# Optimization experiments

Hardware: AMD Instinct MI355X
Metric: run time of the kernel (lower is better)

The kernel has to match this reference:

```python
import jax, jax.numpy as jnp
import numpy as np
from jax import lax

DN = ('NHWC', 'HWIO', 'NHWC')

def _conv(x, k, b, stride=1):
    return lax.conv_general_dilated(x, k, (stride, stride), 'SAME', dimension_numbers=DN) + b

def _tconv(x, k, b):
    return lax.conv_transpose(x, k, (2, 2), 'SAME', dimension_numbers=DN) + b


def setup_inputs() -> dict:
    key = jax.random.key(0)
    ks = jax.random.split(key, 32)
    ki = iter(ks)
    def w(shape, scale=0.05):
        return (jax.random.normal(next(ki), shape, dtype=jnp.float32) * scale)
    inp = {}
    inp['x'] = jax.random.uniform(next(ki), (8, 128, 128, 3), dtype=jnp.float32)
    # encoder
    inp['k1'],  inp['b1']  = w((11, 11, 3, 32)),   jnp.zeros((32,), jnp.float32)
    inp['k1c'], inp['b1c'] = w((3, 3, 32, 32)),    jnp.zeros((32,), jnp.float32)
    inp['k2'],  inp['b2']  = w((11, 11, 32, 64)),  jnp.zeros((64,), jnp.float32)
    inp['k2c'], inp['b2c'] = w((3, 3, 64, 64)),    jnp.zeros((64,), jnp.float32)
    inp['k3'],  inp['b3']  = w((11, 11, 64, 128)), jnp.zeros((128,), jnp.float32)
    inp['k3c'], inp['b3c'] = w((3, 3, 128, 128)),  jnp.zeros((128,), jnp.float32)
    # codebook (codebookSize=256, latent dim 128)
    inp['codebook'] = w((256, 128), 0.1)
    # decoder
    inp['tk1'],  inp['tb1']  = w((5, 5, 128, 64)), jnp.zeros((64,), jnp.float32)
    inp['tk1c'], inp['tb1c'] = w((3, 3, 64, 64)),  jnp.zeros((64,), jnp.float32)
    inp['tk2'],  inp['tb2']  = w((5, 5, 64, 32)),  jnp.zeros((32,), jnp.float32)
    inp['tk2c'], inp['tb2c'] = w((3, 3, 32, 32)),  jnp.zeros((32,), jnp.float32)
    inp['tk3'],  inp['tb3']  = w((5, 5, 32, 32)),  jnp.zeros((32,), jnp.float32)
    inp['tk3c'], inp['tb3c'] = w((3, 3, 32, 3)),   jnp.zeros((3,), jnp.float32)
    return inp


def reference(x, k1, b1, k1c, b1c, k2, b2, k2c, b2c, k3, b3, k3c, b3c,
              codebook, tk1, tb1, tk1c, tb1c, tk2, tb2, tk2c, tb2c,
              tk3, tb3, tk3c, tb3c):
    act = jax.nn.silu  # flax.nnx.swish
    # encoder
    d1 = act(_conv(x, k1, b1, 2))
    d1 = act(_conv(d1, k1c, b1c, 1))
    d2 = act(_conv(d1, k2, b2, 2))
    d2 = act(_conv(d2, k2c, b2c, 1))
    d3 = act(_conv(d2, k3, b3, 2))
    d3 = _conv(d3, k3c, b3c, 1)               # [B, H/8, W/8, 128]
    # vector quantization: squared L2 to each codebook entry
    lat = d3.reshape(-1, 1, 128)              # [N, 1, 128]
    eu_dis = jnp.sum((lat - codebook[None]) ** 2, axis=-1)   # [N, 256]
    idx = jnp.argmin(eu_dis, axis=-1)         # [N]
    quantized = jnp.take(codebook, idx, axis=0).reshape(d3.shape)
    # straight-through estimator
    replaced = lax.stop_gradient(quantized - d3) + d3
    # decoder
    d4 = act(_tconv(replaced, tk1, tb1))
    d4 = act(_conv(d4, tk1c, tb1c, 1))
    d5 = act(_tconv(d4, tk2, tb2))
    d5 = act(_conv(d5, tk2c, tb2c, 1))
    d6 = act(_tconv(d5, tk3, tb3))
    out = _conv(d6, tk3c, tb3c, 1)            # [B, H, W, 3]
    return out
```

## Files before the change

### kernel.cpp

```cpp
#include <hip/hip_runtime.h>

#define DI __device__ __forceinline__
DI float silu_f(float x){ return x * (1.0f/(1.0f+__expf(-x))); }

template<int X> struct LOG2 { static constexpr int v = 1 + LOG2<X/2>::v; };
template<> struct LOG2<1> { static constexpr int v = 0; };

template<int KH,int KW,int STRIDE,int PAD,int CIN,int COUT,int NPIX,
         bool ACT,bool BIAS,int G,int CS,int TOW,int FG>
__global__ __launch_bounds__(256) void conv_k(
    const float* __restrict__ in, const float* __restrict__ w,
    const float* __restrict__ bias, float* __restrict__ out,
    const float* __restrict__ fb, size_t fstr,
    int N,int H,int W,int OH,int OW)
{
  constexpr int CLEN = CIN/G;
  constexpr int COB  = COUT/CS;
  constexpr int COQ  = COB/4;
  constexpr int GSH  = LOG2<G>::v;
  constexpr int CSH  = LOG2<CS>::v;
  constexpr int TAPF = CLEN*COB;
  constexpr bool SALL = (KH*KW*TAPF*4) <= 47*1024;
  constexpr int NTAP = SALL ? KH*KW : KW;
  static_assert(CLEN==3 || (CLEN%4)==0, "ci");
  static_assert(FG==0 || (TOW>0 && CLEN!=3), "fg");
  __shared__ float sw[NTAP*TAPF];
  constexpr int SPAN = (TOW>0) ? (TOW-1)*STRIDE + KW : 1;
  constexpr int ROWS = (TOW>0) ? ((256/COQ)*NPIX)/TOW : 1;
  constexpr int CQ4  = (TOW>0 && CLEN!=3) ? CLEN/4 : 1;
  constexpr int SI_F = (TOW==0) ? 1 : (CLEN==3 ? ROWS*SPAN*3 : ROWS*CQ4*SPAN*4);
  __shared__ float si[SI_F];
  static_assert(TOW==0 || NPIX<=2, "tow npix");
  static_assert(TOW==0 || ((256/COQ)*NPIX) % TOW == 0, "rows");

  const int g  = blockIdx.x & (G-1);
  const int cs = (blockIdx.x >> GSH) & (CS-1);
  const int bx = blockIdx.x >> (GSH+CSH);
  const int total = N*OH*OW;
  if (G>1) out += (size_t)g * total * COUT;
  const int ci_off  = g*CLEN;
  const int co_base = cs*COB;

  int idx = bx*256 + (int)threadIdx.x;
  int cq = idx % COQ;
  int pg = idx / COQ;
  int co = cq*4;
  int gco = co_base + co;
  int p0 = pg*NPIX;

  float acc[NPIX][4] = {};
  int iy0[NPIX], ix0[NPIX]; const float* base[NPIX]; bool pv[NPIX];
#pragma unroll
  for (int t=0;t<NPIX;t++){
    int p=p0+t; pv[t]=(p<total); int pp=pv[t]?p:0;
    int ox=pp%OW; int r=pp/OW; int oy=r%OH; int n=r/OH;
    iy0[t]=oy*STRIDE-PAD; ix0[t]=ox*STRIDE-PAD;
    base[t]=in+(size_t)n*H*W*CIN + ci_off;
  }

  auto stage = [&](int tap0){
    constexpr int TQ = TAPF/4;
    constexpr int V  = NTAP*TQ;
    for (int v=threadIdx.x; v<V; v+=256){
      int tap = v / TQ; int rem = v - tap*TQ;
      float4 q;
      if constexpr (CS==1){
        const float4* src = (const float4*)(w + ((size_t)(tap0+tap)*CIN + ci_off)*COUT);
        q = src[rem];
      } else if constexpr (CLEN==3){
        int ci = rem / (COB/4); int r2 = rem - ci*(COB/4);
        q = *(const float4*)(w + ((size_t)(tap0+tap)*CIN + ci)*COUT
                               + co_base + r2*4);
      } else {
        int ci = rem / (COB/4); int r2 = rem - ci*(COB/4);
        q = *(const float4*)(w + ((size_t)(tap0+tap)*CIN + ci_off + ci)*COUT
                               + co_base + r2*4);
      }
      *(float4*)(sw + (size_t)tap*TAPF + rem*4) = q;
    }
  };

  if constexpr (SALL){
    stage(0);
    __syncthreads();
  }

  if constexpr (TOW>0){
    const int pb0 = bx * ((256/COQ)*NPIX);
    const int r0  = pb0 / TOW;
    const int oy0 = r0 % OH;
    const int n0  = r0 / OH;
    int myrow[NPIX], oxl[NPIX];
#pragma unroll
    for (int t=0;t<NPIX;t++){
      int pl = p0 + t - pb0;
      myrow[t] = pl / TOW;
      oxl[t]   = pl - myrow[t]*TOW;
    }

    for (int ky=0; ky<KH; ky++){
      __syncthreads();
      if constexpr (!SALL) stage(ky*KW);
      if constexpr (CLEN==3){
        constexpr int INS = ROWS*SPAN;
        for (int v=(int)threadIdx.x; v<INS; v+=256){
          int r  = v / SPAN;
          int ixo= v - r*SPAN;
          int iy = (oy0+r)*STRIDE - PAD + ky;
          int ix = ixo - PAD;
          bool ok = iy>=0 && iy<H && ix>=0 && ix<W;
          const float* ip = in + ((size_t)(n0*H+iy)*W + ix)*CIN;
          si[v*3+0] = ok?ip[0]:0.f;
          si[v*3+1] = ok?ip[1]:0.f;
          si[v*3+2] = ok?ip[2]:0.f;
        }
      } else {
        constexpr int INQ = ROWS*CQ4*SPAN;
        for (int v=(int)threadIdx.x; v<INQ; v+=256){
          int r  = v / (CQ4*SPAN);
          int rm = v - r*(CQ4*SPAN);
          int q  = rm / SPAN;
          int ixo= rm - q*SPAN;
          int iy = (oy0+r)*STRIDE - PAD + ky;
          int ix = ixo - PAD;
          bool ok = iy>=0 && iy<H && ix>=0 && ix<W;
          float4 val = make_float4(0.f,0.f,0.f,0.f);
          if (ok){
            size_t off = ((size_t)(n0*H+iy)*W + ix)*CIN + ci_off + q*4;
            if constexpr (FG>0){
              float a[4]; *(float4*)a = *(const float4*)(in + off);
#pragma unroll
              for (int g2=1; g2<FG; g2++){
                float b[4]; *(float4*)b = *(const float4*)(in + (size_t)g2*fstr + off);
#pragma unroll
                for (int j=0;j<4;j++) a[j]+=b[j];
              }
              float bb[4]; *(float4*)bb = *(const float4*)(fb + ci_off + q*4);
#pragma unroll
              for (int j=0;j<4;j++) a[j] = silu_f(a[j]+bb[j]);
              val = *(float4*)a;
            } else {
              val = *(const float4*)(in + off);
            }
          }
          *(float4*)&si[(size_t)v*4] = val;
        }
      }
      __syncthreads();
      const float* swr = SALL ? sw + (size_t)ky*KW*TAPF : sw;
      for (int kx=0; kx<KW; kx++){
        const float* swt = swr + (size_t)kx*TAPF;
        if constexpr (CLEN==3){
          float wv[3][4];
          *(float4*)wv[0]=*(const float4*)(swt + 0*COB + co);
          *(float4*)wv[1]=*(const float4*)(swt + 1*COB + co);
          *(float4*)wv[2]=*(const float4*)(swt + 2*COB + co);
#pragma unroll
          for (int t=0;t<NPIX;t++){
            const float* sp = &si[(size_t)(myrow[t]*SPAN + oxl[t]*STRIDE + kx)*3];
            float v0=sp[0], v1=sp[1], v2=sp[2];
#pragma unroll
            for (int j=0;j<4;j++)
              acc[t][j]=fmaf(v0,wv[0][j],fmaf(v1,wv[1][j],fmaf(v2,wv[2][j],acc[t][j])));
          }
        } else {
#pragma unroll 2
          for (int c=0; c<CQ4; c++){
            float wv[4][4];
#pragma unroll
            for (int r=0;r<4;r++)
              *(float4*)wv[r] = *(const float4*)(swt + (c*4+r)*COB + co);
#pragma unroll
            for (int t=0;t<NPIX;t++){
              float va[4];
              *(float4*)va = *(const float4*)&si[(size_t)((myrow[t]*CQ4 + c)*SPAN + oxl[t]*STRIDE + kx)*4];
#pragma unroll
              for (int r=0;r<4;r++)
#pragma unroll
                for (int j=0;j<4;j++)
                  acc[t][j]=fmaf(va[r],wv[r][j],acc[t][j]);
            }
          }
        }
      }
    }
  } else {
    for (int ky=0; ky<KH; ky++){
      if constexpr (!SALL){
        __syncthreads();
        stage(ky*KW);
        __syncthreads();
      }
      const float* swr = SALL ? sw + (size_t)ky*KW*TAPF : sw;
      for (int kx=0; kx<KW; kx++){
        const float* swt = swr + (size_t)kx*TAPF;
        const float* ip[NPIX]; bool ok[NPIX];
#pragma unroll
        for (int t=0;t<NPIX;t++){
          int iy=iy0[t]+ky, ix=ix0[t]+kx;
          ok[t]=pv[t] && iy>=0 && iy<H && ix>=0 && ix<W;
          ip[t]=base[t]+(size_t)(iy*W+ix)*CIN;
        }
        if constexpr (CLEN==3){
          float wv[3][4];
          *(float4*)wv[0]=*(const float4*)(swt + 0*COB + co);
          *(float4*)wv[1]=*(const float4*)(swt + 1*COB + co);
          *(float4*)wv[2]=*(const float4*)(swt + 2*COB + co);
#pragma unroll
          for (int t=0;t<NPIX;t++){
            float v0=ok[t]?ip[t][0]:0.f;
            float v1=ok[t]?ip[t][1]:0.f;
            float v2=ok[t]?ip[t][2]:0.f;
#pragma unroll
            for (int j=0;j<4;j++)
              acc[t][j]=fmaf(v0,wv[0][j],fmaf(v1,wv[1][j],fmaf(v2,wv[2][j],acc[t][j])));
          }
        } else {
#pragma unroll 2
          for (int ci=0; ci<CLEN; ci+=4){
            float wv[4][4];
#pragma unroll
            for (int r=0;r<4;r++)
              *(float4*)wv[r] = *(const float4*)(swt + (ci+r)*COB + co);
#pragma unroll
            for (int t=0;t<NPIX;t++){
              float va[4];
              *(float4*)va = ok[t] ? *(const float4*)(ip[t]+ci)
                                   : make_float4(0.f,0.f,0.f,0.f);
#pragma unroll
              for (int r=0;r<4;r++)
#pragma unroll
                for (int j=0;j<4;j++)
                  acc[t][j]=fmaf(va[r],wv[r][j],acc[t][j]);
            }
          }
        }
      }
    }
  }

  float bv[4]={0.f,0.f,0.f,0.f};
  if constexpr (BIAS) *(float4*)bv = *(const float4*)(bias+gco);
#pragma unroll
  for (int t=0;t<NPIX;t++) if (pv[t]){
    float o[4];
#pragma unroll
    for (int j=0;j<4;j++){
      float v = acc[t][j]+bv[j];
      o[j] = ACT ? silu_f(v) : v;
    }
    *(float4*)(out + (size_t)(p0+t)*COUT + gco) = *(float4*)o;
  }
}

template<int CIN,int COUT,int NPIX,int G,int CS,int IW,bool DIRECT,int FG>
__global__ __launch_bounds__(256) void tconv_rb(
    const float* __restrict__ in, const float* __restrict__ w,
    const float* __restrict__ bias, float* __restrict__ out,
    const float* __restrict__ fb, size_t fstr,
    int N,int H,int W,int OH,int OW)
{
  constexpr int CLEN = CIN/G;
  constexpr int COB  = COUT/CS;
  constexpr int COQ  = COB/4;
  constexpr int GSH  = LOG2<G>::v;
  constexpr int CSH  = LOG2<CS>::v;
  constexpr int TAPF = CLEN*COB;
  constexpr int PPB  = (256/COQ)*NPIX;
  static_assert(PPB % IW == 0, "whole rows");
  constexpr int ROWS_O = PPB/IW;
  constexpr int NRI  = ROWS_O + 2;
  constexpr int SPAN = IW + 2;
  constexpr int CQ4  = CLEN/4;
  __shared__ float sw[9*TAPF];
  __shared__ float si[NRI*CQ4*SPAN*4];

  const int par = blockIdx.x & 3;
  const int py = par>>1, px = par&1;
  const int g  = (blockIdx.x>>2) & (G-1);
  const int cs = (blockIdx.x>>(2+GSH)) & (CS-1);
  const int bx = blockIdx.x >> (2+GSH+CSH);
  const int NKY = py?3:2, NKX = px?3:2;
  const int OHh = OH>>1;
  if (G>1) out += (size_t)g * (size_t)N*OH*OW*COUT;
  const int co_base = cs*COB;

  const int tid = (int)threadIdx.x;
  int idx = bx*256 + tid;
  int cq = idx % COQ;
  int pg = idx / COQ;
  int co = cq*4;
  int p0 = pg*NPIX;
  const int pb0 = bx*PPB;
  const int R0  = pb0 / IW;
  const int oy0 = R0 % OHh;
  const int n0  = R0 / OHh;

  int myrow[NPIX], xx[NPIX];
#pragma unroll
  for (int t=0;t<NPIX;t++){
    int lp = p0 + t - pb0;
    myrow[t] = lp / IW;
    xx[t]    = lp - myrow[t]*IW;
  }

  {
    constexpr int TQ = TAPF/4;
    const int V = NKY*NKX*TQ;
    for (int v=tid; v<V; v+=256){
      int tap = v / TQ; int rem = v - tap*TQ;
      int j = tap / NKX, i = tap - j*NKX;
      int ky = 2*j + (py?0:1), kx = 2*i + (px?0:1);
      int ci = rem / (COB/4); int r2 = rem - ci*(COB/4);
      float4 q = *(const float4*)(w + ((size_t)(ky*5+kx)*CIN + g*CLEN + ci)*COUT
                                    + co_base + r2*4);
      *(float4*)(sw + (size_t)(j*3+i)*TAPF + rem*4) = q;
    }
  }
  {
    constexpr int INQ = NRI*CQ4*SPAN;
    for (int v=tid; v<INQ; v+=256){
      int r  = v / (CQ4*SPAN);
      int rm = v - r*(CQ4*SPAN);
      int q  = rm / SPAN;
      int cc = rm - q*SPAN;
      int iy = oy0 - 1 + r;
      int ix = cc - 1;
      bool ok = iy>=0 && iy<H && ix>=0 && ix<W;
      float4 val = make_float4(0.f,0.f,0.f,0.f);
      if (ok){
        size_t off = ((size_t)(n0*H+iy)*W + ix)*CIN + g*CLEN + q*4;
        if constexpr (FG>0){
          float a[4]; *(float4*)a = *(const float4*)(in + off);
#pragma unroll
          for (int g2=1; g2<FG; g2++){
            float b[4]; *(float4*)b = *(const float4*)(in + (size_t)g2*fstr + off);
#pragma unroll
            for (int j=0;j<4;j++) a[j]+=b[j];
          }
          float bb[4]; *(float4*)bb = *(const float4*)(fb + g*CLEN + q*4);
#pragma unroll
          for (int j=0;j<4;j++) a[j] = silu_f(a[j]+bb[j]);
          val = *(float4*)a;
        } else {
          val = *(const float4*)(in + off);
        }
      }
      *(float4*)&si[(size_t)v*4] = val;
    }
  }
  __syncthreads();

  float acc[NPIX][4] = {};
  for (int j=0;j<NKY;j++){
    for (int i=0;i<NKX;i++){
      const float* swt = sw + (size_t)(j*3+i)*TAPF;
#pragma unroll 2
      for (int c=0;c<CQ4;c++){
        float wv[4][4];
#pragma unroll
        for (int r=0;r<4;r++)
          *(float4*)wv[r] = *(const float4*)(swt + (c*4+r)*COB + co);
#pragma unroll
        for (int t=0;t<NPIX;t++){
          float va[4];
          *(float4*)va = *(const float4*)&si[(size_t)(((myrow[t]+j)*CQ4 + c)*SPAN + (xx[t]+i))*4];
#pragma unroll
          for (int r=0;r<4;r++)
#pragma unroll
            for (int jj=0;jj<4;jj++)
              acc[t][jj]=fmaf(va[r],wv[r][jj],acc[t][jj]);
        }
      }
    }
  }

  float bv[4]={0.f,0.f,0.f,0.f};
  if constexpr (DIRECT) *(float4*)bv = *(const float4*)(bias+co_base+co);
#pragma unroll
  for (int t=0;t<NPIX;t++){
    float o[4];
#pragma unroll
    for (int jj=0;jj<4;jj++){
      float v = acc[t][jj]+bv[jj];
      o[jj] = DIRECT ? silu_f(v) : v;
    }
    *(float4*)(out + (((size_t)n0*OH + (2*(oy0+myrow[t])+py))*OW + (2*xx[t]+px))*COUT + co_base+co) = *(float4*)o;
  }
}

__global__ __launch_bounds__(256) void vq_k(
    const float* __restrict__ p, const float* __restrict__ bias,
    const float* __restrict__ cb, float* __restrict__ q, int NLat)
{
  __shared__ float slat[4][128];
  int wave = threadIdx.x >> 6;
  int lane = threadIdx.x & 63;
  int l = blockIdx.x*4 + wave;
  if (l >= NLat) return;
  const float* p0 = p + (size_t)l*128;
  const float* p1 = p0 + (size_t)NLat*128;
  slat[wave][lane]    = p0[lane]    + p1[lane]    + bias[lane];
  slat[wave][lane+64] = p0[lane+64] + p1[lane+64] + bias[lane+64];

  float bestd = INFINITY; int besti = 0;
  for (int c0=0;c0<256;c0+=64){
    int c = c0 + lane;
    const float* cp = cb + (size_t)c*128;
    float d = 0.f;
#pragma unroll 8
    for (int k=0;k<128;k+=4){
      float4 cv = *reinterpret_cast<const float4*>(cp+k);
      float d0 = slat[wave][k+0]-cv.x;
      float d1 = slat[wave][k+1]-cv.y;
      float d2 = slat[wave][k+2]-cv.z;
      float d3 = slat[wave][k+3]-cv.w;
      d += d0*d0; d += d1*d1; d += d2*d2; d += d3*d3;
    }
    if (d < bestd) { bestd = d; besti = c; }
  }
  for (int off=32; off; off>>=1){
    float od = __shfl_down(bestd, off);
    int   oi = __shfl_down(besti, off);
    if (od < bestd || (od == bestd && oi < besti)) { bestd=od; besti=oi; }
  }
  besti = __shfl(besti, 0);
  const float* cp = cb + (size_t)besti*128;
  float* qp = q + (size_t)l*128;
  qp[lane]    = cp[lane];
  qp[lane+64] = cp[lane+64];
}

__global__ __launch_bounds__(256) void conv_last_k(
    const float* __restrict__ in, const float* __restrict__ w,
    float* __restrict__ p, int N,int H,int W)
{
  int g = blockIdx.x % 3;
  int bx = blockIdx.x / 3;
  int pix = bx*256 + threadIdx.x;
  int total = N*H*W;
  if (pix>=total) return;
  int x = pix % W; int r = pix / W; int y = r % H; int n = r / H;
  float a0=0.f, a1=0.f, a2=0.f;
  int iy = y + g - 1;
  if (iy>=0 && iy<H){
    const float* base = in + ((size_t)n*H + iy)*W*32;
    for (int kx=0;kx<3;kx++){
      int ix=x+kx-1; if(ix<0||ix>=W) continue;
      const float* ip = base + (size_t)ix*32;
      const float* wp = w + (size_t)((g*3+kx)*32)*3;
#pragma unroll
      for (int ci=0;ci<32;ci+=4){
        float va[4]; *(float4*)va = *(const float4*)(ip+ci);
        float wv[12];
        *(float4*)(wv+0) = *(const float4*)(wp+ci*3+0);
        *(float4*)(wv+4) = *(const float4*)(wp+ci*3+4);
        *(float4*)(wv+8) = *(const float4*)(wp+ci*3+8);
#pragma unroll
        for (int r2=0;r2<4;r2++){
          a0 = fmaf(va[r2], wv[r2*3+0], a0);
          a1 = fmaf(va[r2], wv[r2*3+1], a1);
          a2 = fmaf(va[r2], wv[r2*3+2], a2);
        }
      }
    }
  }
  float* pp = p + (size_t)g*total*3 + (size_t)pix*3;
  pp[0]=a0; pp[1]=a1; pp[2]=a2;
}

__global__ __launch_bounds__(256) void reduce_last_k(
    const float* __restrict__ p, const float* __restrict__ bias,
    float* __restrict__ out, int n)
{
  int i = (blockIdx.x*256+threadIdx.x)*4;
  if (i>=n) return;
  float a[4]; *(float4*)a = *(const float4*)(p+i);
#pragma unroll
  for (int g=1; g<3; g++){
    float b[4]; *(float4*)b = *(const float4*)(p+(size_t)g*n+i);
#pragma unroll
    for (int j=0;j<4;j++) a[j]+=b[j];
  }
  float o[4];
#pragma unroll
  for (int j=0;j<4;j++) o[j] = a[j] + bias[(i+j)%3];
  *(float4*)(out+i) = *(float4*)o;
}

extern "C" void kernel_launch(void* const* d_in, const int* in_sizes, int n_in,
                              void* d_out, int out_size, void* d_ws, size_t ws_size,
                              hipStream_t stream) {
  const float* x    = (const float*)d_in[0];
  const float* k1   = (const float*)d_in[1];  const float* b1  = (const float*)d_in[2];
  const float* k1c  = (const float*)d_in[3];  const float* b1c = (const float*)d_in[4];
  const float* k2   = (const float*)d_in[5];  const float* b2  = (const float*)d_in[6];
  const float* k2c  = (const float*)d_in[7];  const float* b2c = (const float*)d_in[8];
  const float* k3   = (const float*)d_in[9];  const float* b3  = (const float*)d_in[10];
  const float* k3c  = (const float*)d_in[11]; const float* b3c = (const float*)d_in[12];
  const float* cb   = (const float*)d_in[13];
  const float* tk1  = (const float*)d_in[14]; const float* tb1  = (const float*)d_in[15];
  const float* tk1c = (const float*)d_in[16]; const float* tb1c = (const float*)d_in[17];
  const float* tk2  = (const float*)d_in[18]; const float* tb2  = (const float*)d_in[19];
  const float* tk2c = (const float*)d_in[20]; const float* tb2c = (const float*)d_in[21];
  const float* tk3  = (const float*)d_in[22]; const float* tb3  = (const float*)d_in[23];
  const float* tk3c = (const float*)d_in[24]; const float* tb3c = (const float*)d_in[25];
  float* out = (float*)d_out;

  float* S  = (float*)d_ws;
  float* W0 = S;
  float* W1 = S + 1048576;
  float* PA = S + 2097152;
  float* PB = S + 3145728;
  float* PC = S + 2097152;
  float* PD = S + 2097152;
  float* PE = S + 4194304;
  float* PF = S + 2097152;
  float* PG = S + 2097152;
  dim3 blk(256);

  conv_k<11,11,2,4,  3, 32,2,true ,true ,1,2,64,0><<< 512,blk,0,stream>>>(x,  k1,  b1,  W0, nullptr,0, 8,128,128,64,64);
  conv_k< 3, 3,1,1, 32, 32,2,true ,true ,1,2,64,0><<< 512,blk,0,stream>>>(W0, k1c, b1c, W1, nullptr,0, 8,64,64,64,64);
  conv_k<11,11,2,4, 32, 64,2,false,false,2,2,32,0><<< 512,blk,0,stream>>>(W1, k2,  nullptr, PA, nullptr,0, 8,64,64,32,32);
  conv_k< 3, 3,1,1, 64, 64,1,true ,true ,1,2,32,2><<< 512,blk,0,stream>>>(PA, k2c, b2c, W0, b2,524288, 8,32,32,32,32);
  conv_k<11,11,2,4, 64,128,2,false,false,4,4,16,0><<< 512,blk,0,stream>>>(W0, k3,  nullptr, PB, nullptr,0, 8,32,32,16,16);
  conv_k< 3, 3,1,1,128,128,1,false,false,2,4,16,4><<< 512,blk,0,stream>>>(PB, k3c, nullptr, PC, b3,262144, 8,16,16,16,16);
  vq_k<<<512,blk,0,stream>>>(PC, b3c, cb, W1, 2048);
  tconv_rb<128,64,1,4,2,16,false,0><<<2048,blk,0,stream>>>(W1, tk1, nullptr, PD, nullptr,0, 8,16,16,32,32);
  conv_k< 3, 3,1,1, 64, 64,2,false,false,2,4,32,4><<< 512,blk,0,stream>>>(PD, tk1c, nullptr, PE, tb1,524288, 8,32,32,32,32);
  tconv_rb< 64,32,1,2,1,32,false,2><<<2048,blk,0,stream>>>(PE, tk2, nullptr, PF, tb1c,524288, 8,32,32,64,64);
  conv_k< 3, 3,1,1, 32, 32,2,true ,true ,1,2,64,2><<< 512,blk,0,stream>>>(PF, tk2c, tb2c, W1, tb2,1048576, 8,64,64,64,64);
  tconv_rb< 32,32,1,1,2,64,true ,0><<<4096,blk,0,stream>>>(W1, tk3, tb3, PG, nullptr,0, 8,64,64,128,128);
  conv_last_k<<<1536,blk,0,stream>>>(PG, tk3c, S, 8,128,128);
  reduce_last_k<<<384,blk,0,stream>>>(S, tb3c, out, 393216);
}
```

Measured before the change: 451.1 us.

## Double-buffer weight and input staging across kernel rows in tiled conv

For tiled convolutions whose weights do not fit entirely in shared memory, the weights and input rows for the next kernel row are staged into a second shared buffer while the current row is computed. This replaces two barriers per kernel row with one and lets global loads overlap with FMA work. The cost is doubled shared-memory usage, which can reduce occupancy.

```diff
diff --git a/kernel.cpp b/kernel.cpp
--- a/kernel.cpp
+++ b/kernel.cpp
@@ -22,14 +22,15 @@
   constexpr int TAPF = CLEN*COB;
   constexpr bool SALL = (KH*KW*TAPF*4) <= 47*1024;
   constexpr int NTAP = SALL ? KH*KW : KW;
+  constexpr bool DBUF = (TOW>0) && !SALL && (CLEN!=3) && (FG==0);
   static_assert(CLEN==3 || (CLEN%4)==0, "ci");
   static_assert(FG==0 || (TOW>0 && CLEN!=3), "fg");
-  __shared__ float sw[NTAP*TAPF];
+  __shared__ float sw[(DBUF?2:1)*NTAP*TAPF];
   constexpr int SPAN = (TOW>0) ? (TOW-1)*STRIDE + KW : 1;
   constexpr int ROWS = (TOW>0) ? ((256/COQ)*NPIX)/TOW : 1;
   constexpr int CQ4  = (TOW>0 && CLEN!=3) ? CLEN/4 : 1;
   constexpr int SI_F = (TOW==0) ? 1 : (CLEN==3 ? ROWS*SPAN*3 : ROWS*CQ4*SPAN*4);
-  __shared__ float si[SI_F];
+  __shared__ float si[(DBUF?2:1)*SI_F];
   static_assert(TOW==0 || NPIX<=2, "tow npix");
   static_assert(TOW==0 || ((256/COQ)*NPIX) % TOW == 0, "rows");
 
@@ -58,7 +59,7 @@
     base[t]=in+(size_t)n*H*W*CIN + ci_off;
   }
 
-  auto stage = [&](int tap0){
+  auto stage = [&](int tap0, float* dst){
     constexpr int TQ = TAPF/4;
     constexpr int V  = NTAP*TQ;
     for (int v=threadIdx.x; v<V; v+=256){
@@ -76,12 +77,12 @@
         q = *(const float4*)(w + ((size_t)(tap0+tap)*CIN + ci_off + ci)*COUT
                                + co_base + r2*4);
       }
-      *(float4*)(sw + (size_t)tap*TAPF + rem*4) = q;
+      *(float4*)(dst + (size_t)tap*TAPF + rem*4) = q;
     }
   };
 
   if constexpr (SALL){
-    stage(0);
+    stage(0, sw);
     __syncthreads();
   }
 
@@ -98,9 +99,7 @@
       oxl[t]   = pl - myrow[t]*TOW;
     }
 
-    for (int ky=0; ky<KH; ky++){
-      __syncthreads();
-      if constexpr (!SALL) stage(ky*KW);
+    auto stage_in = [&](int ky, float* dsi){
       if constexpr (CLEN==3){
         constexpr int INS = ROWS*SPAN;
         for (int v=(int)threadIdx.x; v<INS; v+=256){
@@ -110,9 +109,9 @@
           int ix = ixo - PAD;
           bool ok = iy>=0 && iy<H && ix>=0 && ix<W;
           const float* ip = in + ((size_t)(n0*H+iy)*W + ix)*CIN;
-          si[v*3+0] = ok?ip[0]:0.f;
-          si[v*3+1] = ok?ip[1]:0.f;
-          si[v*3+2] = ok?ip[2]:0.f;
+          dsi[v*3+0] = ok?ip[0]:0.f;
+          dsi[v*3+1] = ok?ip[1]:0.f;
+          dsi[v*3+2] = ok?ip[2]:0.f;
         }
       } else {
         constexpr int INQ = ROWS*CQ4*SPAN;
@@ -143,11 +142,12 @@
               val = *(const float4*)(in + off);
             }
           }
-          *(float4*)&si[(size_t)v*4] = val;
-        }
-      }
-      __syncthreads();
-      const float* swr = SALL ? sw + (size_t)ky*KW*TAPF : sw;
+          *(float4*)&dsi[(size_t)v*4] = val;
+        }
+      }
+    };
+
+    auto compute_ky = [&](const float* swr, const float* sib){
       for (int kx=0; kx<KW; kx++){
         const float* swt = swr + (size_t)kx*TAPF;
         if constexpr (CLEN==3){
@@ -157,7 +157,7 @@
           *(float4*)wv[2]=*(const float4*)(swt + 2*COB + co);
 #pragma unroll
           for (int t=0;t<NPIX;t++){
-            const float* sp = &si[(size_t)(myrow[t]*SPAN + oxl[t]*STRIDE + kx)*3];
+            const float* sp = &sib[(size_t)(myrow[t]*SPAN + oxl[t]*STRIDE + kx)*3];
             float v0=sp[0], v1=sp[1], v2=sp[2];
 #pragma unroll
             for (int j=0;j<4;j++)
@@ -173,7 +173,7 @@
 #pragma unroll
             for (int t=0;t<NPIX;t++){
               float va[4];
-              *(float4*)va = *(const float4*)&si[(size_t)((myrow[t]*CQ4 + c)*SPAN + oxl[t]*STRIDE + kx)*4];
+              *(float4*)va = *(const float4*)&sib[(size_t)((myrow[t]*CQ4 + c)*SPAN + oxl[t]*STRIDE + kx)*4];
 #pragma unroll
               for (int r=0;r<4;r++)
 #pragma unroll
@@ -183,12 +183,36 @@
           }
         }
       }
+    };
+
+    if constexpr (DBUF){
+      stage(0, sw);
+      stage_in(0, si);
+      __syncthreads();
+      for (int ky=0; ky<KH; ky++){
+        const int cur = ky&1, nxt = cur^1;
+        if (ky+1<KH){
+          stage((ky+1)*KW, sw + (size_t)nxt*NTAP*TAPF);
+          stage_in(ky+1, si + (size_t)nxt*SI_F);
+        }
+        compute_ky(sw + (size_t)cur*NTAP*TAPF, si + (size_t)cur*SI_F);
+        __syncthreads();
+      }
+    } else {
+      for (int ky=0; ky<KH; ky++){
+        __syncthreads();
+        if constexpr (!SALL) stage(ky*KW, sw);
+        stage_in(ky, si);
+        __syncthreads();
+        const float* swr = SALL ? sw + (size_t)ky*KW*TAPF : sw;
+        compute_ky(swr, si);
+      }
     }
   } else {
     for (int ky=0; ky<KH; ky++){
       if constexpr (!SALL){
         __syncthreads();
-        stage(ky*KW);
+        stage(ky*KW, sw);
         __syncthreads();
       }
       const float* swr = SALL ? sw + (size_t)ky*KW*TAPF : sw;
```

Measured after the change: 451.0 us. Within noise of the previous version (-0.0%).
